# Kernel tuning notes

Hardware: AMD Instinct MI355X
Metric: run time of the kernel (lower is better)

The kernel has to match this reference:

```python
import jax, jax.numpy as jnp
import numpy as np

DIM = 640
HEADS = 10
HEAD_DIM = DIM // HEADS
SCALE = DIM ** (-0.5)  # note: module scales by full dim**-0.5, not head_dim


def setup_inputs() -> dict:
    key = jax.random.key(0)
    ks = jax.random.split(key, 5)
    B, N = 16, 1024
    x = jax.random.normal(ks[0], (B, N, DIM), dtype=jnp.float32)
    w_qkv = jax.random.normal(ks[1], (DIM, 3 * DIM), dtype=jnp.float32) * (DIM ** -0.5)
    b_qkv = jnp.zeros((3 * DIM,), dtype=jnp.float32)
    w_out = jax.random.normal(ks[2], (DIM, DIM), dtype=jnp.float32) * (DIM ** -0.5)
    b_out = jnp.zeros((DIM,), dtype=jnp.float32)
    return {"x": x, "w_qkv": w_qkv, "b_qkv": b_qkv, "w_out": w_out, "b_out": b_out}


def reference(x, w_qkv, b_qkv, w_out, b_out):
    B, N, _ = x.shape
    qkv = x @ w_qkv + b_qkv                     # [B, N, 3*DIM]
    qkv = qkv.reshape(B, N, 3, HEADS, HEAD_DIM)
    q, k, v = qkv[:, :, 0], qkv[:, :, 1], qkv[:, :, 2]   # [B, N, H, Dh]
    # scores: QK^T scaled by dim**-0.5 (module's normfactor)
    scores = jnp.einsum('bihd,bjhd->bhij', q, k) * SCALE  # [B, H, N, N]
    attn = jax.nn.softmax(scores, axis=-1)
    out = jnp.einsum('bhij,bjhd->bihd', attn, v)          # [B, N, H, Dh]
    out = out.reshape(B, N, DIM)
    return out @ w_out + b_out
```

## Files before the change

### kernel.cpp

```cpp
#include <hip/hip_runtime.h>

#define DIM 640
#define NHEADS 10
#define HDIM 64
#define SEQ 1024
#define BATCH 16
#define MROWS (BATCH * SEQ)
#define QKVN (3 * DIM)
#define NBH (BATCH * NHEADS)

typedef float f32x4 __attribute__((ext_vector_type(4)));
typedef __bf16 bf16x8 __attribute__((ext_vector_type(8)));

#define SM_C 0.057027536f

__device__ __forceinline__ unsigned short f2b(float f) {
  union { __bf16 h; unsigned short u; } v;
  v.h = (__bf16)f;
  return v.u;
}

__device__ __forceinline__ f32x4 mfma16(bf16x8 a, bf16x8 b, f32x4 c) {
  return __builtin_amdgcn_mfma_f32_16x16x32_bf16(a, b, c, 0, 0, 0);
}

typedef __attribute__((address_space(3))) unsigned int as3_u32;
typedef const __attribute__((address_space(1))) unsigned int as1_u32;
__device__ __forceinline__ void glds16(const unsigned short* g, unsigned short* l) {
  __builtin_amdgcn_global_load_lds((as1_u32*)g, (as3_u32*)l, 16, 0, 0);
}

__device__ __forceinline__ int kv_remap(int y) {
  return 32 * (y >> 5) + 8 * ((y & 15) >> 2) + (y & 3) + 4 * ((y >> 4) & 1);
}

__global__ __launch_bounds__(256) void convert_x(
    const float* __restrict__ X, unsigned short* __restrict__ xb) {
  int i = (blockIdx.x * 256 + threadIdx.x) * 4;
  float4 v = *(const float4*)(X + i);
  ushort4 s;
  s.x = f2b(v.x); s.y = f2b(v.y); s.z = f2b(v.z); s.w = f2b(v.w);
  *(ushort4*)(xb + i) = s;
}

__global__ __launch_bounds__(256) void transpose_w(
    const float* __restrict__ W, unsigned short* __restrict__ Wt, int R, int C) {
  __shared__ int tile[32][33];
  const int tx = threadIdx.x & 31, ty = threadIdx.x >> 5;
  const int c0 = blockIdx.x * 32, r0 = blockIdx.y * 32;
#pragma unroll
  for (int i = 0; i < 4; ++i)
    tile[ty + 8 * i][tx] = f2b(W[(r0 + ty + 8 * i) * C + c0 + tx]);
  __syncthreads();
#pragma unroll
  for (int i = 0; i < 4; ++i)
    Wt[(c0 + ty + 8 * i) * R + r0 + tx] = (unsigned short)tile[tx][ty + 8 * i];
}

__global__ __launch_bounds__(256) void qkv_gemm(
    const unsigned short* __restrict__ A, const unsigned short* __restrict__ Bt,
    const float* __restrict__ bias,
    unsigned short* __restrict__ qw, unsigned short* __restrict__ kw,
    unsigned short* __restrict__ vtw) {
  __shared__ __attribute__((aligned(16))) unsigned short As[128 * 64];
  __shared__ __attribute__((aligned(16))) unsigned short Bs[128 * 64];
  const int t = threadIdx.x;
  const int lane = t & 63, w = t >> 6;
  const int quad = lane >> 4, cl = lane & 15;
  const int nxb = gridDim.x;
  const int flatb = blockIdx.y * nxb + blockIdx.x;
  const int cpx = (nxb * gridDim.y) >> 3;
  const int swz = (flatb & 7) * cpx + (flatb >> 3);
  const int m0 = (swz / nxb) * 128, n0 = (swz % nxb) * 128;
  const int wr = (w >> 1) * 64, wc = (w & 1) * 64;

  const int r8 = lane >> 3;
  const int sw = ((lane & 7) ^ r8) * 8;
  const unsigned short* asrc = A + (size_t)(m0 + w * 32 + r8) * DIM + sw;
  const unsigned short* bsrc = Bt + (size_t)(n0 + w * 32 + r8) * DIM + sw;

  const int x = cl & 7;
  const int aoff0 = (wr + cl) * 64 + (quad ^ x) * 8;
  const int aoff1 = (wr + cl) * 64 + ((4 + quad) ^ x) * 8;
  const int boff0 = (wc + cl) * 64 + (quad ^ x) * 8;
  const int boff1 = (wc + cl) * 64 + ((4 + quad) ^ x) * 8;

  f32x4 acc[4][4];
#pragma unroll
  for (int i = 0; i < 4; ++i)
#pragma unroll
    for (int j = 0; j < 4; ++j) acc[i][j] = (f32x4){0.f, 0.f, 0.f, 0.f};

  for (int kt = 0; kt < DIM / 64; ++kt) {
    __syncthreads();
#pragma unroll
    for (int i = 0; i < 4; ++i) {
      glds16(asrc + (size_t)i * 8 * DIM, &As[(w * 32 + i * 8) * 64]);
      glds16(bsrc + (size_t)i * 8 * DIM, &Bs[(w * 32 + i * 8) * 64]);
    }
    asrc += 64; bsrc += 64;
    __syncthreads();
#pragma unroll
    for (int ks = 0; ks < 2; ++ks) {
      const int ao = ks ? aoff1 : aoff0, bo = ks ? boff1 : boff0;
      bf16x8 af[4], bfr[4];
#pragma unroll
      for (int i = 0; i < 4; ++i) af[i] = *(const bf16x8*)&As[ao + i * 1024];
#pragma unroll
      for (int j = 0; j < 4; ++j) bfr[j] = *(const bf16x8*)&Bs[bo + j * 1024];
#pragma unroll
      for (int i = 0; i < 4; ++i)
#pragma unroll
        for (int j = 0; j < 4; ++j) acc[i][j] = mfma16(af[i], bfr[j], acc[i][j]);
    }
  }

  const int sec = n0 / DIM;
  unsigned short* qk = (sec == 0) ? qw : kw;
  const float sc = (sec == 0) ? SM_C : 1.0f;
#pragma unroll
  for (int j = 0; j < 4; ++j) {
    int cc = n0 + wc + j * 16 + cl;
    int cr = cc - sec * DIM;
    int h = cr >> 6, d = cr & 63;
    float bv = bias[cc];
#pragma unroll
    for (int i = 0; i < 4; ++i) {
      int rbase = m0 + wr + i * 16 + quad * 4;
      int b = rbase >> 10, n = rbase & 1023;
      int bh = b * NHEADS + h;
      if (sec < 2) {
        size_t base = ((size_t)bh * SEQ + n) * HDIM + d;
#pragma unroll
        for (int r = 0; r < 4; ++r)
          qk[base + (size_t)r * HDIM] = f2b((acc[i][j][r] + bv) * sc);
      } else {
        ushort4 s;
        s.x = f2b(acc[i][j][0] + bv);
        s.y = f2b(acc[i][j][1] + bv);
        s.z = f2b(acc[i][j][2] + bv);
        s.w = f2b(acc[i][j][3] + bv);
        *(ushort4*)(vtw + ((size_t)bh * HDIM + d) * SEQ + n) = s;
      }
    }
  }
}

__global__ __launch_bounds__(256) void attn_kernel(
    const unsigned short* __restrict__ qw, const unsigned short* __restrict__ kw,
    const unsigned short* __restrict__ vtw, unsigned short* __restrict__ out) {
  __shared__ __attribute__((aligned(16))) unsigned short Ks[2][64 * 64];
  __shared__ __attribute__((aligned(16))) unsigned short Vs[2][64 * 64];
  const int t = threadIdx.x;
  const int lane = t & 63, w = t >> 6;
  const int quad = lane >> 4, cl = lane & 15;
  const int flat = blockIdx.x;
  const int bh = flat % NBH;
  const int qb = flat / NBH;
  const size_t qkbase = (size_t)bh * SEQ * HDIM;
  const size_t vbase  = (size_t)bh * HDIM * SEQ;

  const int r8 = lane >> 3;
  const int sw = ((lane & 7) ^ r8) * 8;
  const int y0 = w * 16 + r8;
  const int y1 = w * 16 + 8 + r8;
  const unsigned short* ksrc0 = kw + qkbase + (size_t)kv_remap(y0) * HDIM + sw;
  const unsigned short* ksrc1 = kw + qkbase + (size_t)kv_remap(y1) * HDIM + sw;
  const unsigned short* vsrc  = vtw + vbase + (size_t)(w * 16 + r8) * SEQ + sw;

  const int x = cl & 7;
  const int koff0 = cl * 64 + (quad ^ x) * 8;
  const int koff1 = cl * 64 + ((4 + quad) ^ x) * 8;

  bf16x8 aq[2][2];
#pragma unroll
  for (int i = 0; i < 2; ++i) {
    const unsigned short* qp =
        qw + qkbase + (size_t)(qb * 128 + w * 32 + i * 16 + cl) * HDIM;
    aq[i][0] = *(const bf16x8*)(qp + quad * 8);
    aq[i][1] = *(const bf16x8*)(qp + 32 + quad * 8);
  }

  union { unsigned short u[8]; bf16x8 v; } ow;
#pragma unroll
  for (int j = 0; j < 8; ++j) ow.u[j] = 0x3F80;
  const bf16x8 ones8 = ow.v;

  f32x4 o_acc[2][4];
#pragma unroll
  for (int i = 0; i < 2; ++i)
#pragma unroll
    for (int dt = 0; dt < 4; ++dt) o_acc[i][dt] = (f32x4){0.f, 0.f, 0.f, 0.f};
  f32x4 o1[2];
  o1[0] = (f32x4){0.f, 0.f, 0.f, 0.f};
  o1[1] = (f32x4){0.f, 0.f, 0.f, 0.f};

  glds16(ksrc0, &Ks[0][(w * 16) * 64]);
  glds16(ksrc1, &Ks[0][(w * 16 + 8) * 64]);
  glds16(vsrc,           &Vs[0][(w * 16) * 64]);
  glds16(vsrc + 8 * SEQ, &Vs[0][(w * 16 + 8) * 64]);

  for (int kt = 0; kt < 16; ++kt) {
    const int cur = kt & 1, nxt = cur ^ 1;
    __syncthreads();

    if (kt < 15) {
      const unsigned short* kp0 = ksrc0 + (size_t)(kt + 1) * 64 * HDIM;
      const unsigned short* kp1 = ksrc1 + (size_t)(kt + 1) * 64 * HDIM;
      const unsigned short* vp  = vsrc + (kt + 1) * 64;
      glds16(kp0, &Ks[nxt][(w * 16) * 64]);
      glds16(kp1, &Ks[nxt][(w * 16 + 8) * 64]);
      glds16(vp,           &Vs[nxt][(w * 16) * 64]);
      glds16(vp + 8 * SEQ, &Vs[nxt][(w * 16 + 8) * 64]);
    }

    const unsigned short* Kc = &Ks[cur][0];
    const unsigned short* Vc = &Vs[cur][0];

    __builtin_amdgcn_s_setprio(1);

    bf16x8 pfr[2][2];
#pragma unroll
    for (int c = 0; c < 2; ++c) {
      bf16x8 ka0 = *(const bf16x8*)&Kc[koff0 + c * 2048];
      bf16x8 ka1 = *(const bf16x8*)&Kc[koff1 + c * 2048];
      bf16x8 kb0 = *(const bf16x8*)&Kc[koff0 + c * 2048 + 1024];
      bf16x8 kb1 = *(const bf16x8*)&Kc[koff1 + c * 2048 + 1024];
#pragma unroll
      for (int i = 0; i < 2; ++i) {
        f32x4 zA = (f32x4){0.f, 0.f, 0.f, 0.f};
        zA = mfma16(ka0, aq[i][0], zA);
        zA = mfma16(ka1, aq[i][1], zA);
        f32x4 zB = (f32x4){0.f, 0.f, 0.f, 0.f};
        zB = mfma16(kb0, aq[i][0], zB);
        zB = mfma16(kb1, aq[i][1], zB);
        union { unsigned short u[8]; bf16x8 v; } pk;
#pragma unroll
        for (int r = 0; r < 4; ++r) {
          pk.u[r]     = f2b(__builtin_amdgcn_exp2f(zA[r]));
          pk.u[4 + r] = f2b(__builtin_amdgcn_exp2f(zB[r]));
        }
        pfr[i][c] = pk.v;
        o1[i] = mfma16(pfr[i][c], ones8, o1[i]);
      }
    }

#pragma unroll
    for (int dt = 0; dt < 4; ++dt) {
      const int vrow = dt * 16 + cl;
      const int vx = vrow & 7;
#pragma unroll
      for (int c = 0; c < 2; ++c) {
        bf16x8 bv = *(const bf16x8*)&Vc[vrow * 64 + ((4 * c + quad) ^ vx) * 8];
#pragma unroll
        for (int i = 0; i < 2; ++i)
          o_acc[i][dt] = mfma16(pfr[i][c], bv, o_acc[i][dt]);
      }
    }

    __builtin_amdgcn_s_setprio(0);
  }

  const int b = bh / NHEADS, h = bh % NHEADS;
#pragma unroll
  for (int i = 0; i < 2; ++i)
#pragma unroll
    for (int r = 0; r < 4; ++r) {
      float inv = 1.f / o1[i][r];
      int row = b * SEQ + qb * 128 + w * 32 + i * 16 + quad * 4 + r;
#pragma unroll
      for (int dt = 0; dt < 4; ++dt)
        out[(size_t)row * DIM + h * HDIM + dt * 16 + cl] =
            f2b(o_acc[i][dt][r] * inv);
    }
}

__global__ __launch_bounds__(256) void out_gemm(
    const unsigned short* __restrict__ A, const unsigned short* __restrict__ Bt,
    const float* __restrict__ bias, float* __restrict__ C) {
  __shared__ __attribute__((aligned(16))) unsigned short As[128 * 64];
  __shared__ __attribute__((aligned(16))) unsigned short Bs[128 * 64];
  const int t = threadIdx.x;
  const int lane = t & 63, w = t >> 6;
  const int quad = lane >> 4, cl = lane & 15;
  const int nxb = gridDim.x;
  const int flatb = blockIdx.y * nxb + blockIdx.x;
  const int cpx = (nxb * gridDim.y) >> 3;
  const int swz = (flatb & 7) * cpx + (flatb >> 3);
  const int m0 = (swz / nxb) * 128, n0 = (swz % nxb) * 128;
  const int wr = (w >> 1) * 64, wc = (w & 1) * 64;

  const int r8 = lane >> 3;
  const int sw = ((lane & 7) ^ r8) * 8;
  const unsigned short* asrc = A + (size_t)(m0 + w * 32 + r8) * DIM + sw;
  const unsigned short* bsrc = Bt + (size_t)(n0 + w * 32 + r8) * DIM + sw;

  const int x = cl & 7;
  const int aoff0 = (wr + cl) * 64 + (quad ^ x) * 8;
  const int aoff1 = (wr + cl) * 64 + ((4 + quad) ^ x) * 8;
  const int boff0 = (wc + cl) * 64 + (quad ^ x) * 8;
  const int boff1 = (wc + cl) * 64 + ((4 + quad) ^ x) * 8;

  f32x4 acc[4][4];
#pragma unroll
  for (int i = 0; i < 4; ++i)
#pragma unroll
    for (int j = 0; j < 4; ++j) acc[i][j] = (f32x4){0.f, 0.f, 0.f, 0.f};

  for (int kt = 0; kt < DIM / 64; ++kt) {
    __syncthreads();
#pragma unroll
    for (int i = 0; i < 4; ++i) {
      glds16(asrc + (size_t)i * 8 * DIM, &As[(w * 32 + i * 8) * 64]);
      glds16(bsrc + (size_t)i * 8 * DIM, &Bs[(w * 32 + i * 8) * 64]);
    }
    asrc += 64; bsrc += 64;
    __syncthreads();
#pragma unroll
    for (int ks = 0; ks < 2; ++ks) {
      const int ao = ks ? aoff1 : aoff0, bo = ks ? boff1 : boff0;
      bf16x8 af[4], bfr[4];
#pragma unroll
      for (int i = 0; i < 4; ++i) af[i] = *(const bf16x8*)&As[ao + i * 1024];
#pragma unroll
      for (int j = 0; j < 4; ++j) bfr[j] = *(const bf16x8*)&Bs[bo + j * 1024];
#pragma unroll
      for (int i = 0; i < 4; ++i)
#pragma unroll
        for (int j = 0; j < 4; ++j) acc[i][j] = mfma16(af[i], bfr[j], acc[i][j]);
    }
  }
#pragma unroll
  for (int j = 0; j < 4; ++j) {
    int cc = n0 + wc + j * 16 + cl;
    float bv = bias[cc];
#pragma unroll
    for (int i = 0; i < 4; ++i) {
#pragma unroll
      for (int r = 0; r < 4; ++r) {
        int rr = m0 + wr + i * 16 + quad * 4 + r;
        C[(size_t)rr * DIM + cc] = acc[i][j][r] + bv;
      }
    }
  }
}

extern "C" void kernel_launch(void* const* d_in, const int* in_sizes, int n_in,
                              void* d_out, int out_size, void* d_ws, size_t ws_size,
                              hipStream_t stream) {
  const float* x     = (const float*)d_in[0];
  const float* w_qkv = (const float*)d_in[1];
  const float* b_qkv = (const float*)d_in[2];
  const float* w_out = (const float*)d_in[3];
  const float* b_out = (const float*)d_in[4];
  float* out = (float*)d_out;

  unsigned short* ws = (unsigned short*)d_ws;
  unsigned short* xb      = ws;
  unsigned short* wt_qkv  = ws + 10485760;
  unsigned short* wt_out  = wt_qkv + 1228800;
  unsigned short* qw      = wt_out + 409600;
  unsigned short* kw      = qw + 10485760;
  unsigned short* vtw     = kw + 10485760;
  unsigned short* attn_ws = xb;

  convert_x<<<MROWS * DIM / 1024, 256, 0, stream>>>(x, xb);
  transpose_w<<<dim3(QKVN / 32, DIM / 32), 256, 0, stream>>>(w_qkv, wt_qkv, DIM, QKVN);
  transpose_w<<<dim3(DIM / 32, DIM / 32), 256, 0, stream>>>(w_out, wt_out, DIM, DIM);
  qkv_gemm<<<dim3(QKVN / 128, MROWS / 128), 256, 0, stream>>>(xb, wt_qkv, b_qkv, qw, kw, vtw);
  attn_kernel<<<dim3(NBH * (SEQ / 128)), 256, 0, stream>>>(qw, kw, vtw, attn_ws);
  out_gemm<<<dim3(DIM / 128, MROWS / 128), 256, 0, stream>>>(attn_ws, wt_out, b_out, out);
}
```

Measured before the change: 240.7 us.

## Double-buffer LDS tiles in QKV and output GEMMs to overlap loads with MFMA

Both projection GEMMs now keep two LDS buffers for the A and B tiles. The next k-tile is staged with async global-to-LDS loads while MFMAs run on the current one, and only one barrier is left per iteration instead of two. The aim is to hide global load latency behind compute. In exchange, LDS per block doubles to 64KB, which can lower occupancy. The overlap may also be lost if the compiler inserts conservative vmcnt waits before the LDS reads.

```diff
diff --git a/kernel.cpp b/kernel.cpp
--- a/kernel.cpp
+++ b/kernel.cpp
@@ -62,8 +62,8 @@
     const float* __restrict__ bias,
     unsigned short* __restrict__ qw, unsigned short* __restrict__ kw,
     unsigned short* __restrict__ vtw) {
-  __shared__ __attribute__((aligned(16))) unsigned short As[128 * 64];
-  __shared__ __attribute__((aligned(16))) unsigned short Bs[128 * 64];
+  __shared__ __attribute__((aligned(16))) unsigned short As[2][128 * 64];
+  __shared__ __attribute__((aligned(16))) unsigned short Bs[2][128 * 64];
   const int t = threadIdx.x;
   const int lane = t & 63, w = t >> 6;
   const int quad = lane >> 4, cl = lane & 15;
@@ -91,27 +91,40 @@
 #pragma unroll
     for (int j = 0; j < 4; ++j) acc[i][j] = (f32x4){0.f, 0.f, 0.f, 0.f};
 
+  auto stage = [&](int buf, int kt) {
+    const unsigned short* a_ = asrc + (size_t)kt * 64;
+    const unsigned short* b_ = bsrc + (size_t)kt * 64;
+#pragma unroll
+    for (int i = 0; i < 4; ++i) {
+      glds16(a_ + (size_t)i * 8 * DIM, &As[buf][(w * 32 + i * 8) * 64]);
+      glds16(b_ + (size_t)i * 8 * DIM, &Bs[buf][(w * 32 + i * 8) * 64]);
+    }
+  };
+
+  stage(0, 0);
+  __syncthreads();
+
+  int cur = 0;
   for (int kt = 0; kt < DIM / 64; ++kt) {
-    __syncthreads();
-#pragma unroll
-    for (int i = 0; i < 4; ++i) {
-      glds16(asrc + (size_t)i * 8 * DIM, &As[(w * 32 + i * 8) * 64]);
-      glds16(bsrc + (size_t)i * 8 * DIM, &Bs[(w * 32 + i * 8) * 64]);
-    }
-    asrc += 64; bsrc += 64;
-    __syncthreads();
+    if (kt + 1 < DIM / 64) stage(cur ^ 1, kt + 1);
+    const unsigned short* Ap = &As[cur][0];
+    const unsigned short* Bp = &Bs[cur][0];
 #pragma unroll
     for (int ks = 0; ks < 2; ++ks) {
       const int ao = ks ? aoff1 : aoff0, bo = ks ? boff1 : boff0;
       bf16x8 af[4], bfr[4];
 #pragma unroll
-      for (int i = 0; i < 4; ++i) af[i] = *(const bf16x8*)&As[ao + i * 1024];
-#pragma unroll
-      for (int j = 0; j < 4; ++j) bfr[j] = *(const bf16x8*)&Bs[bo + j * 1024];
+      for (int i = 0; i < 4; ++i) af[i] = *(const bf16x8*)&Ap[ao + i * 1024];
+#pragma unroll
+      for (int j = 0; j < 4; ++j) bfr[j] = *(const bf16x8*)&Bp[bo + j * 1024];
 #pragma unroll
       for (int i = 0; i < 4; ++i)
 #pragma unroll
         for (int j = 0; j < 4; ++j) acc[i][j] = mfma16(af[i], bfr[j], acc[i][j]);
+    }
+    if (kt + 1 < DIM / 64) {
+      __syncthreads();
+      cur ^= 1;
     }
   }
 
@@ -278,8 +291,8 @@
 __global__ __launch_bounds__(256) void out_gemm(
     const unsigned short* __restrict__ A, const unsigned short* __restrict__ Bt,
     const float* __restrict__ bias, float* __restrict__ C) {
-  __shared__ __attribute__((aligned(16))) unsigned short As[128 * 64];
-  __shared__ __attribute__((aligned(16))) unsigned short Bs[128 * 64];
+  __shared__ __attribute__((aligned(16))) unsigned short As[2][128 * 64];
+  __shared__ __attribute__((aligned(16))) unsigned short Bs[2][128 * 64];
   const int t = threadIdx.x;
   const int lane = t & 63, w = t >> 6;
   const int quad = lane >> 4, cl = lane & 15;
@@ -307,27 +320,40 @@
 #pragma unroll
     for (int j = 0; j < 4; ++j) acc[i][j] = (f32x4){0.f, 0.f, 0.f, 0.f};
 
+  auto stage = [&](int buf, int kt) {
+    const unsigned short* a_ = asrc + (size_t)kt * 64;
+    const unsigned short* b_ = bsrc + (size_t)kt * 64;
+#pragma unroll
+    for (int i = 0; i < 4; ++i) {
+      glds16(a_ + (size_t)i * 8 * DIM, &As[buf][(w * 32 + i * 8) * 64]);
+      glds16(b_ + (size_t)i * 8 * DIM, &Bs[buf][(w * 32 + i * 8) * 64]);
+    }
+  };
+
+  stage(0, 0);
+  __syncthreads();
+
+  int cur = 0;
   for (int kt = 0; kt < DIM / 64; ++kt) {
-    __syncthreads();
-#pragma unroll
-    for (int i = 0; i < 4; ++i) {
-      glds16(asrc + (size_t)i * 8 * DIM, &As[(w * 32 + i * 8) * 64]);
-      glds16(bsrc + (size_t)i * 8 * DIM, &Bs[(w * 32 + i * 8) * 64]);
-    }
-    asrc += 64; bsrc += 64;
-    __syncthreads();
+    if (kt + 1 < DIM / 64) stage(cur ^ 1, kt + 1);
+    const unsigned short* Ap = &As[cur][0];
+    const unsigned short* Bp = &Bs[cur][0];
 #pragma unroll
     for (int ks = 0; ks < 2; ++ks) {
       const int ao = ks ? aoff1 : aoff0, bo = ks ? boff1 : boff0;
       bf16x8 af[4], bfr[4];
 #pragma unroll
-      for (int i = 0; i < 4; ++i) af[i] = *(const bf16x8*)&As[ao + i * 1024];
-#pragma unroll
-      for (int j = 0; j < 4; ++j) bfr[j] = *(const bf16x8*)&Bs[bo + j * 1024];
+      for (int i = 0; i < 4; ++i) af[i] = *(const bf16x8*)&Ap[ao + i * 1024];
+#pragma unroll
+      for (int j = 0; j < 4; ++j) bfr[j] = *(const bf16x8*)&Bp[bo + j * 1024];
 #pragma unroll
       for (int i = 0; i < 4; ++i)
 #pragma unroll
         for (int j = 0; j < 4; ++j) acc[i][j] = mfma16(af[i], bfr[j], acc[i][j]);
+    }
+    if (kt + 1 < DIM / 64) {
+      __syncthreads();
+      cur ^= 1;
     }
   }
 #pragma unroll
```

Result: slower. 246.6 us (+2.5%).

## Triple-buffer K/V tiles with prefetch distance two and partial vmcnt waits

Applied to the files above, without the earlier changes.

Grows the shared-memory K/V staging from double to triple buffering and issues loads two tiles ahead. A partial s_waitcnt vmcnt(4) followed by a raw barrier replaces __syncthreads, so loads for the next tile can stay in flight while the current tile is computed. This is meant to hide more global-load latency, at the cost of extra LDS per block (possibly lower occupancy). It also relies on exact vmcnt accounting, so any other outstanding vector memory ops could break correctness.

```diff
diff --git a/kernel.cpp b/kernel.cpp
--- a/kernel.cpp
+++ b/kernel.cpp
@@ -149,8 +149,8 @@
 __global__ __launch_bounds__(256) void attn_kernel(
     const unsigned short* __restrict__ qw, const unsigned short* __restrict__ kw,
     const unsigned short* __restrict__ vtw, unsigned short* __restrict__ out) {
-  __shared__ __attribute__((aligned(16))) unsigned short Ks[2][64 * 64];
-  __shared__ __attribute__((aligned(16))) unsigned short Vs[2][64 * 64];
+  __shared__ __attribute__((aligned(16))) unsigned short Ks[3][64 * 64];
+  __shared__ __attribute__((aligned(16))) unsigned short Vs[3][64 * 64];
   const int t = threadIdx.x;
   const int lane = t & 63, w = t >> 6;
   const int quad = lane >> 4, cl = lane & 15;
@@ -195,25 +195,27 @@
   o1[0] = (f32x4){0.f, 0.f, 0.f, 0.f};
   o1[1] = (f32x4){0.f, 0.f, 0.f, 0.f};
 
-  glds16(ksrc0, &Ks[0][(w * 16) * 64]);
-  glds16(ksrc1, &Ks[0][(w * 16 + 8) * 64]);
-  glds16(vsrc,           &Vs[0][(w * 16) * 64]);
-  glds16(vsrc + 8 * SEQ, &Vs[0][(w * 16 + 8) * 64]);
+  auto stageKV = [&](int b, int tile) {
+    const unsigned short* kp0 = ksrc0 + (size_t)tile * 64 * HDIM;
+    const unsigned short* kp1 = ksrc1 + (size_t)tile * 64 * HDIM;
+    const unsigned short* vp  = vsrc + tile * 64;
+    glds16(kp0,          &Ks[b][(w * 16) * 64]);
+    glds16(kp1,          &Ks[b][(w * 16 + 8) * 64]);
+    glds16(vp,           &Vs[b][(w * 16) * 64]);
+    glds16(vp + 8 * SEQ, &Vs[b][(w * 16 + 8) * 64]);
+  };
+
+  stageKV(0, 0);
+  stageKV(1, 1);
 
   for (int kt = 0; kt < 16; ++kt) {
-    const int cur = kt & 1, nxt = cur ^ 1;
-    __syncthreads();
-
-    if (kt < 15) {
-      const unsigned short* kp0 = ksrc0 + (size_t)(kt + 1) * 64 * HDIM;
-      const unsigned short* kp1 = ksrc1 + (size_t)(kt + 1) * 64 * HDIM;
-      const unsigned short* vp  = vsrc + (kt + 1) * 64;
-      glds16(kp0, &Ks[nxt][(w * 16) * 64]);
-      glds16(kp1, &Ks[nxt][(w * 16 + 8) * 64]);
-      glds16(vp,           &Vs[nxt][(w * 16) * 64]);
-      glds16(vp + 8 * SEQ, &Vs[nxt][(w * 16 + 8) * 64]);
-    }
-
+    if (kt < 15) asm volatile("s_waitcnt vmcnt(4)" ::: "memory");
+    else         asm volatile("s_waitcnt vmcnt(0)" ::: "memory");
+    __builtin_amdgcn_s_barrier();
+
+    if (kt + 2 < 16) stageKV((kt + 2) % 3, kt + 2);
+
+    const int cur = kt % 3;
     const unsigned short* Kc = &Ks[cur][0];
     const unsigned short* Vc = &Vs[cur][0];
 
```

New measurement: 233.5 us. 3.0% less time.
